# Performance work log

Hardware: AMD Instinct MI355X
Metric: run time of the kernel (lower is better)

The kernel has to match this reference:

```python
import jax, jax.numpy as jnp
import numpy as np

HIDDEN = 512
VOCAB = 50000
SEQ = 4096


def setup_inputs() -> dict:
    key = jax.random.key(0)
    ks = jax.random.split(key, 8)
    s = 1.0 / np.sqrt(HIDDEN)
    return {
        "x": jax.random.randint(ks[0], (1, SEQ), 0, VOCAB, dtype=jnp.int64),
        "target": jax.random.uniform(ks[1], (1, 1), dtype=jnp.float32),
        "emb": jax.random.normal(ks[2], (VOCAB, HIDDEN), dtype=jnp.float32),
        "w_ih": jax.random.uniform(ks[3], (3 * HIDDEN, HIDDEN), minval=-s, maxval=s, dtype=jnp.float32),
        "w_hh": jax.random.uniform(ks[4], (3 * HIDDEN, HIDDEN), minval=-s, maxval=s, dtype=jnp.float32),
        "b_ih": jax.random.uniform(ks[5], (3 * HIDDEN,), minval=-s, maxval=s, dtype=jnp.float32),
        "b_hh": jax.random.uniform(ks[6], (3 * HIDDEN,), minval=-s, maxval=s, dtype=jnp.float32),
        "dec_w": jax.random.uniform(ks[7], (1, HIDDEN), minval=-s, maxval=s, dtype=jnp.float32),
        "dec_b": jnp.zeros((1,), dtype=jnp.float32),
    }


def reference(x, target, emb, w_ih, w_hh, b_ih, b_hh, dec_w, dec_b):
    H = emb.shape[1]
    # embedding lookup for whole sequence (dropout in eval mode = identity)
    xe = emb[x[0]]                       # [S, H]
    # precompute input-side gate projections for all timesteps
    gx = xe @ w_ih.T + b_ih              # [S, 3H]

    def step(h, gx_t):
        gh = h @ w_hh.T + b_hh           # [3H]
        r = jax.nn.sigmoid(gx_t[:H] + gh[:H])
        z = jax.nn.sigmoid(gx_t[H:2 * H] + gh[H:2 * H])
        n = jnp.tanh(gx_t[2 * H:] + r * gh[2 * H:])
        h_new = (1.0 - z) * n + z * h
        return h_new, None

    h0 = jnp.zeros((H,), dtype=xe.dtype)
    hT, _ = jax.lax.scan(step, h0, gx)   # final hidden state [H]

    # decoder logit, then sigmoid + BCE (stable log-sigmoid form)
    logit = hT @ dec_w[0] + dec_b[0]     # scalar
    t = target[0, 0]
    loss = -(t * jax.nn.log_sigmoid(logit) + (1.0 - t) * jax.nn.log_sigmoid(-logit))
    return loss
```

## Files before the change

kernel.cpp:

```cpp
#include <hip/hip_runtime.h>

constexpr int S   = 4096;
constexpr int H   = 512;
constexpr int G3  = 1536;
constexpr int NWG = 32;

__global__ __launch_bounds__(256) void gemm_gx(
    const int* __restrict__ x, const float* __restrict__ emb,
    const float* __restrict__ w_ih, const float* __restrict__ b_ih,
    float* __restrict__ gx)
{
    __shared__ alignas(16) float As[128][36];
    __shared__ alignas(16) float Bs[32][132];

    const int tid  = threadIdx.x;
    const int row0 = (blockIdx.x / 12) * 128;
    const int col0 = (blockIdx.x % 12) * 128;
    const int tx   = tid & 15;
    const int ty   = tid >> 4;

    float acc[8][8] = {};

    for (int k0 = 0; k0 < H; k0 += 32) {
        #pragma unroll
        for (int p = 0; p < 4; ++p) {
            const int rl = (tid >> 3) + 32 * p;
            const int kk = (tid & 7) * 4;
            const int xi = x[row0 + rl];
            const float4 va = *reinterpret_cast<const float4*>(
                emb + (size_t)xi * H + k0 + kk);
            *reinterpret_cast<float4*>(&As[rl][kk]) = va;

            const float4 vb = *reinterpret_cast<const float4*>(
                w_ih + (size_t)(col0 + rl) * H + k0 + kk);
            Bs[kk + 0][rl] = vb.x; Bs[kk + 1][rl] = vb.y;
            Bs[kk + 2][rl] = vb.z; Bs[kk + 3][rl] = vb.w;
        }
        __syncthreads();

        #pragma unroll
        for (int kk = 0; kk < 32; ++kk) {
            float a[8], b[8];
            #pragma unroll
            for (int q = 0; q < 4; ++q) {
                a[q]     = As[ty * 4 + q][kk];
                a[4 + q] = As[ty * 4 + 64 + q][kk];
            }
            const float4 b0 = *reinterpret_cast<const float4*>(&Bs[kk][tx * 4]);
            const float4 b1 = *reinterpret_cast<const float4*>(&Bs[kk][tx * 4 + 64]);
            b[0]=b0.x; b[1]=b0.y; b[2]=b0.z; b[3]=b0.w;
            b[4]=b1.x; b[5]=b1.y; b[6]=b1.z; b[7]=b1.w;
            #pragma unroll
            for (int ri = 0; ri < 8; ++ri)
                #pragma unroll
                for (int ci = 0; ci < 8; ++ci)
                    acc[ri][ci] = fmaf(a[ri], b[ci], acc[ri][ci]);
        }
        __syncthreads();
    }

    float bi[8];
    #pragma unroll
    for (int q = 0; q < 4; ++q) {
        bi[q]     = b_ih[col0 + tx * 4 + q];
        bi[4 + q] = b_ih[col0 + tx * 4 + 64 + q];
    }
    #pragma unroll
    for (int ri = 0; ri < 8; ++ri) {
        const int rr = row0 + ty * 4 + (ri & 3) + ((ri >> 2) << 6);
        float4 o0, o1;
        o0.x = acc[ri][0] + bi[0]; o0.y = acc[ri][1] + bi[1];
        o0.z = acc[ri][2] + bi[2]; o0.w = acc[ri][3] + bi[3];
        o1.x = acc[ri][4] + bi[4]; o1.y = acc[ri][5] + bi[5];
        o1.z = acc[ri][6] + bi[6]; o1.w = acc[ri][7] + bi[7];
        *reinterpret_cast<float4*>(gx + (size_t)rr * G3 + col0 + tx * 4)      = o0;
        *reinterpret_cast<float4*>(gx + (size_t)rr * G3 + col0 + tx * 4 + 64) = o1;
    }
}

__global__ __launch_bounds__(256, 1) void gru_scan(
    const float* __restrict__ gx,
    const float* __restrict__ w_hh,
    const float* __restrict__ b_hh,
    const float* __restrict__ dec_w,
    const float* __restrict__ dec_b,
    const float* __restrict__ target,
    unsigned long long* __restrict__ hbuf,
    float* __restrict__ out)
{
    __shared__ float h_lds[H];

    const int k   = blockIdx.x;
    const int tid = threadIdx.x;
    const int l   = tid & 15;
    const int g   = tid >> 4;
    const int i   = k * 16 + g;

    float4 wr[8], wz[8], wn[8];
    #pragma unroll
    for (int j = 0; j < 8; ++j) {
        const int c = 4 * l + 64 * j;
        wr[j] = *reinterpret_cast<const float4*>(w_hh + (size_t)i * H + c);
        wz[j] = *reinterpret_cast<const float4*>(w_hh + (size_t)(H + i) * H + c);
        wn[j] = *reinterpret_cast<const float4*>(w_hh + (size_t)(2 * H + i) * H + c);
    }
    const float bhr = b_hh[i], bhz = b_hh[H + i], bhn = b_hh[2 * H + i];

    float gxr = 0.f, gxz = 0.f, gxn = 0.f;
    if (l == 0) { gxr = gx[i]; gxz = gx[H + i]; gxn = gx[2 * H + i]; }

    const int e0 = tid, e1 = tid + 256;

    for (int s = 0; s < S; ++s) {
        if (s == 0) {
            h_lds[e0] = 0.f; h_lds[e1] = 0.f;
        } else {
            unsigned long long* src = hbuf + (size_t)(s & 1) * H;
            unsigned long long v0 = 0, v1 = 0;
            bool d0 = false, d1 = false;
            const unsigned tg = (unsigned)s;
            while (true) {
                if (!d0) { v0 = __hip_atomic_load(src + e0, __ATOMIC_RELAXED,
                                                  __HIP_MEMORY_SCOPE_AGENT);
                           d0 = (unsigned)(v0 >> 32) == tg; }
                if (!d1) { v1 = __hip_atomic_load(src + e1, __ATOMIC_RELAXED,
                                                  __HIP_MEMORY_SCOPE_AGENT);
                           d1 = (unsigned)(v1 >> 32) == tg; }
                if (d0 && d1) break;
            }
            h_lds[e0] = __uint_as_float((unsigned)v0);
            h_lds[e1] = __uint_as_float((unsigned)v1);
        }
        __syncthreads();

        const float hp = h_lds[i];

        float ar = 0.f, az = 0.f, an = 0.f;
        #pragma unroll
        for (int j = 0; j < 8; ++j) {
            const float4 hv =
                *reinterpret_cast<const float4*>(&h_lds[64 * j + 4 * l]);
            ar = fmaf(wr[j].x, hv.x, fmaf(wr[j].y, hv.y,
                 fmaf(wr[j].z, hv.z, fmaf(wr[j].w, hv.w, ar))));
            az = fmaf(wz[j].x, hv.x, fmaf(wz[j].y, hv.y,
                 fmaf(wz[j].z, hv.z, fmaf(wz[j].w, hv.w, az))));
            an = fmaf(wn[j].x, hv.x, fmaf(wn[j].y, hv.y,
                 fmaf(wn[j].z, hv.z, fmaf(wn[j].w, hv.w, an))));
        }
        #pragma unroll
        for (int m = 8; m >= 1; m >>= 1) {
            ar += __shfl_xor(ar, m);
            az += __shfl_xor(az, m);
            an += __shfl_xor(an, m);
        }

        if (l == 0) {
            const float r  = 1.f / (1.f + __expf(-(gxr + ar + bhr)));
            const float z  = 1.f / (1.f + __expf(-(gxz + az + bhz)));
            const float nn = tanhf(gxn + r * (an + bhn));
            const float hnew = (1.f - z) * nn + z * hp;
            const unsigned long long pv =
                ((unsigned long long)(unsigned)(s + 1) << 32) |
                (unsigned long long)__float_as_uint(hnew);
            __hip_atomic_store(hbuf + (size_t)((s + 1) & 1) * H + i, pv,
                               __ATOMIC_RELAXED, __HIP_MEMORY_SCOPE_AGENT);
            const int sn = (s + 1 < S) ? (s + 1) : s;
            gxr = gx[(size_t)sn * G3 + i];
            gxz = gx[(size_t)sn * G3 + H + i];
            gxn = gx[(size_t)sn * G3 + 2 * H + i];
        }
        __syncthreads();
    }

    if (k == 0) {
        unsigned long long* src = hbuf;
        unsigned long long v0 = 0, v1 = 0;
        bool d0 = false, d1 = false;
        while (true) {
            if (!d0) { v0 = __hip_atomic_load(src + e0, __ATOMIC_RELAXED,
                                              __HIP_MEMORY_SCOPE_AGENT);
                       d0 = (unsigned)(v0 >> 32) == (unsigned)S; }
            if (!d1) { v1 = __hip_atomic_load(src + e1, __ATOMIC_RELAXED,
                                              __HIP_MEMORY_SCOPE_AGENT);
                       d1 = (unsigned)(v1 >> 32) == (unsigned)S; }
            if (d0 && d1) break;
        }
        h_lds[e0] = __uint_as_float((unsigned)v0);
        h_lds[e1] = __uint_as_float((unsigned)v1);
        __syncthreads();

        if (tid < 64) {
            float p = 0.f;
            #pragma unroll
            for (int j = 0; j < 8; ++j)
                p = fmaf(h_lds[tid + 64 * j], dec_w[tid + 64 * j], p);
            #pragma unroll
            for (int m = 32; m >= 1; m >>= 1) p += __shfl_xor(p, m);
            if (tid == 0) {
                const float xl = p + dec_b[0];
                const float t  = target[0];
                const float loss = fmaxf(xl, 0.f) - xl * t +
                                   log1pf(__expf(-fabsf(xl)));
                out[0] = loss;
            }
        }
    }
}

extern "C" void kernel_launch(void* const* d_in, const int* in_sizes, int n_in,
                              void* d_out, int out_size, void* d_ws, size_t ws_size,
                              hipStream_t stream) {
    const int*   x      = (const int*)d_in[0];
    const float* target = (const float*)d_in[1];
    const float* emb    = (const float*)d_in[2];
    const float* w_ih   = (const float*)d_in[3];
    const float* w_hh   = (const float*)d_in[4];
    const float* b_ih   = (const float*)d_in[5];
    const float* b_hh   = (const float*)d_in[6];
    const float* dec_w  = (const float*)d_in[7];
    const float* dec_b  = (const float*)d_in[8];
    float*       out    = (float*)d_out;

    float* gx = (float*)d_ws;
    unsigned long long* hbuf =
        (unsigned long long*)((char*)d_ws + (size_t)S * G3 * sizeof(float));

    hipMemsetAsync(hbuf, 0, 2 * H * sizeof(unsigned long long), stream);

    gemm_gx<<<dim3(32 * 12), dim3(256), 0, stream>>>(x, emb, w_ih, b_ih, gx);
    gru_scan<<<dim3(NWG), dim3(256), 0, stream>>>(gx, w_hh, b_hh, dec_w, dec_b,
                                                  target, hbuf, out);
}
```

Measured before the change: 8.090 ms.

## Co-locate scan workgroups on one XCD and exchange hidden state through L2

The scan kernel now launches 256 workgroups and keeps only every eighth one, so that under round-robin XCD dispatch all 32 active workgroups should sit on the same XCD. Each step publishes h both to an L2-coherent buffer, using sc0 inline-asm stores and loads, and to the original agent-scope buffer. Consumers poll the L2 buffer with vectorized 16-byte loads and fall back to the agent-scope buffer after a bounded spin. The trailing per-step __syncthreads is also dropped, aiming to cut the per-timestep cross-XCD communication latency that bounds the 4096-step recurrence. This relies on an undocumented workgroup-to-XCD placement and on the fallback path if that assumption fails.

```diff
diff --git a/kernel.cpp b/kernel.cpp
--- a/kernel.cpp
+++ b/kernel.cpp
@@ -1,9 +1,22 @@
 #include <hip/hip_runtime.h>
 
-constexpr int S   = 4096;
-constexpr int H   = 512;
-constexpr int G3  = 1536;
-constexpr int NWG = 32;
+constexpr int S    = 4096;
+constexpr int H    = 512;
+constexpr int G3   = 1536;
+constexpr int NWG  = 32;
+constexpr int GRID = 256;
+constexpr int FAST_BOUND = 16384;
+
+__device__ inline uint4 ld4_l2(const void* p) {
+    uint4 v;
+    asm volatile("global_load_dwordx4 %0, %1, off sc0\n\ts_waitcnt vmcnt(0)"
+                 : "=v"(v) : "v"(p) : "memory");
+    return v;
+}
+__device__ inline void st2_l2(void* p, unsigned long long v) {
+    asm volatile("global_store_dwordx2 %0, %1, off sc0"
+                 :: "v"(p), "v"(v) : "memory");
+}
 
 __global__ __launch_bounds__(256) void gemm_gx(
     const int* __restrict__ x, const float* __restrict__ emb,
@@ -85,51 +98,75 @@
     const float* __restrict__ dec_w,
     const float* __restrict__ dec_b,
     const float* __restrict__ target,
-    unsigned long long* __restrict__ hbuf,
+    unsigned long long* __restrict__ hl2,
+    unsigned long long* __restrict__ hml,
     float* __restrict__ out)
 {
+    const int bid = blockIdx.x;
+    if ((bid & 7) != 0) return;
+    const int k = bid >> 3;
+
     __shared__ float h_lds[H];
 
-    const int k   = blockIdx.x;
     const int tid = threadIdx.x;
     const int l   = tid & 15;
     const int g   = tid >> 4;
     const int i   = k * 16 + g;
+    const int e0  = 2 * tid, e1 = 2 * tid + 1;
 
     float4 wr[8], wz[8], wn[8];
     #pragma unroll
     for (int j = 0; j < 8; ++j) {
-        const int c = 4 * l + 64 * j;
-        wr[j] = *reinterpret_cast<const float4*>(w_hh + (size_t)i * H + c);
-        wz[j] = *reinterpret_cast<const float4*>(w_hh + (size_t)(H + i) * H + c);
-        wn[j] = *reinterpret_cast<const float4*>(w_hh + (size_t)(2 * H + i) * H + c);
+        const volatile float* pr =
+            (const volatile float*)(w_hh + (size_t)i * H + 4 * l + 64 * j);
+        const volatile float* pz = pr + (size_t)H * H;
+        const volatile float* pn = pz + (size_t)H * H;
+        wr[j] = make_float4(pr[0], pr[1], pr[2], pr[3]);
+        wz[j] = make_float4(pz[0], pz[1], pz[2], pz[3]);
+        wn[j] = make_float4(pn[0], pn[1], pn[2], pn[3]);
     }
     const float bhr = b_hh[i], bhz = b_hh[H + i], bhn = b_hh[2 * H + i];
 
     float gxr = 0.f, gxz = 0.f, gxn = 0.f;
     if (l == 0) { gxr = gx[i]; gxz = gx[H + i]; gxn = gx[2 * H + i]; }
 
-    const int e0 = tid, e1 = tid + 256;
+    bool use_mall = false;
 
     for (int s = 0; s < S; ++s) {
         if (s == 0) {
             h_lds[e0] = 0.f; h_lds[e1] = 0.f;
         } else {
-            unsigned long long* src = hbuf + (size_t)(s & 1) * H;
-            unsigned long long v0 = 0, v1 = 0;
-            bool d0 = false, d1 = false;
-            const unsigned tg = (unsigned)s;
-            while (true) {
-                if (!d0) { v0 = __hip_atomic_load(src + e0, __ATOMIC_RELAXED,
-                                                  __HIP_MEMORY_SCOPE_AGENT);
-                           d0 = (unsigned)(v0 >> 32) == tg; }
-                if (!d1) { v1 = __hip_atomic_load(src + e1, __ATOMIC_RELAXED,
-                                                  __HIP_MEMORY_SCOPE_AGENT);
-                           d1 = (unsigned)(v1 >> 32) == tg; }
-                if (d0 && d1) break;
-            }
-            h_lds[e0] = __uint_as_float((unsigned)v0);
-            h_lds[e1] = __uint_as_float((unsigned)v1);
+            const unsigned tg   = (unsigned)s;
+            const size_t   boff = (size_t)(s & 1) * H;
+            unsigned x0, x1;
+            bool got = false;
+            if (!use_mall) {
+                const uint4* src =
+                    reinterpret_cast<const uint4*>(hl2 + boff) + tid;
+                uint4 v = ld4_l2(src);
+                int it = 0;
+                while (!(v.y == tg && v.w == tg) && it < FAST_BOUND) {
+                    ++it; v = ld4_l2(src);
+                }
+                if (v.y == tg && v.w == tg) { x0 = v.x; x1 = v.z; got = true; }
+                else use_mall = true;
+            }
+            if (!got) {
+                unsigned long long* src = hml + boff;
+                unsigned long long v0 = 0, v1 = 0;
+                bool d0 = false, d1 = false;
+                while (!(d0 && d1)) {
+                    if (!d0) { v0 = __hip_atomic_load(src + e0, __ATOMIC_RELAXED,
+                                                      __HIP_MEMORY_SCOPE_AGENT);
+                               d0 = (unsigned)(v0 >> 32) == tg; }
+                    if (!d1) { v1 = __hip_atomic_load(src + e1, __ATOMIC_RELAXED,
+                                                      __HIP_MEMORY_SCOPE_AGENT);
+                               d1 = (unsigned)(v1 >> 32) == tg; }
+                }
+                x0 = (unsigned)v0; x1 = (unsigned)v1;
+            }
+            h_lds[e0] = __uint_as_float(x0);
+            h_lds[e1] = __uint_as_float(x1);
         }
         __syncthreads();
 
@@ -162,31 +199,46 @@
             const unsigned long long pv =
                 ((unsigned long long)(unsigned)(s + 1) << 32) |
                 (unsigned long long)__float_as_uint(hnew);
-            __hip_atomic_store(hbuf + (size_t)((s + 1) & 1) * H + i, pv,
+            const size_t dsts = (size_t)((s + 1) & 1) * H + i;
+            st2_l2(hl2 + dsts, pv);
+            __hip_atomic_store(hml + dsts, pv,
                                __ATOMIC_RELAXED, __HIP_MEMORY_SCOPE_AGENT);
             const int sn = (s + 1 < S) ? (s + 1) : s;
             gxr = gx[(size_t)sn * G3 + i];
             gxz = gx[(size_t)sn * G3 + H + i];
             gxn = gx[(size_t)sn * G3 + 2 * H + i];
         }
-        __syncthreads();
     }
 
     if (k == 0) {
-        unsigned long long* src = hbuf;
-        unsigned long long v0 = 0, v1 = 0;
-        bool d0 = false, d1 = false;
-        while (true) {
-            if (!d0) { v0 = __hip_atomic_load(src + e0, __ATOMIC_RELAXED,
-                                              __HIP_MEMORY_SCOPE_AGENT);
-                       d0 = (unsigned)(v0 >> 32) == (unsigned)S; }
-            if (!d1) { v1 = __hip_atomic_load(src + e1, __ATOMIC_RELAXED,
-                                              __HIP_MEMORY_SCOPE_AGENT);
-                       d1 = (unsigned)(v1 >> 32) == (unsigned)S; }
-            if (d0 && d1) break;
-        }
-        h_lds[e0] = __uint_as_float((unsigned)v0);
-        h_lds[e1] = __uint_as_float((unsigned)v1);
+        const unsigned tg = (unsigned)S;
+        unsigned x0, x1;
+        bool got = false;
+        if (!use_mall) {
+            const uint4* src = reinterpret_cast<const uint4*>(hl2) + tid;
+            uint4 v = ld4_l2(src);
+            int it = 0;
+            while (!(v.y == tg && v.w == tg) && it < FAST_BOUND) {
+                ++it; v = ld4_l2(src);
+            }
+            if (v.y == tg && v.w == tg) { x0 = v.x; x1 = v.z; got = true; }
+            else use_mall = true;
+        }
+        if (!got) {
+            unsigned long long v0 = 0, v1 = 0;
+            bool d0 = false, d1 = false;
+            while (!(d0 && d1)) {
+                if (!d0) { v0 = __hip_atomic_load(hml + e0, __ATOMIC_RELAXED,
+                                                  __HIP_MEMORY_SCOPE_AGENT);
+                           d0 = (unsigned)(v0 >> 32) == tg; }
+                if (!d1) { v1 = __hip_atomic_load(hml + e1, __ATOMIC_RELAXED,
+                                                  __HIP_MEMORY_SCOPE_AGENT);
+                           d1 = (unsigned)(v1 >> 32) == tg; }
+            }
+            x0 = (unsigned)v0; x1 = (unsigned)v1;
+        }
+        h_lds[e0] = __uint_as_float(x0);
+        h_lds[e1] = __uint_as_float(x1);
         __syncthreads();
 
         if (tid < 64) {
@@ -222,12 +274,13 @@
     float*       out    = (float*)d_out;
 
     float* gx = (float*)d_ws;
-    unsigned long long* hbuf =
+    unsigned long long* hl2 =
         (unsigned long long*)((char*)d_ws + (size_t)S * G3 * sizeof(float));
-
-    hipMemsetAsync(hbuf, 0, 2 * H * sizeof(unsigned long long), stream);
+    unsigned long long* hml = hl2 + 2 * H;
+
+    hipMemsetAsync(hl2, 0, 4 * H * sizeof(unsigned long long), stream);
 
     gemm_gx<<<dim3(32 * 12), dim3(256), 0, stream>>>(x, emb, w_ih, b_ih, gx);
-    gru_scan<<<dim3(NWG), dim3(256), 0, stream>>>(gx, w_hh, b_hh, dec_w, dec_b,
-                                                  target, hbuf, out);
-}
+    gru_scan<<<dim3(GRID), dim3(256), 0, stream>>>(gx, w_hh, b_hh, dec_w, dec_b,
+                                                   target, hl2, hml, out);
+}
```

New measurement: 25.23 ms. 212% more time.

## Poll hidden state with wide system-coherent loads and stage recurrent weights in LDS

Applied to the files above, without the earlier changes.

The per-step inter-workgroup handoff now polls 16 bytes per thread (two tagged entries) using an inline-asm global_load_dwordx4 with sc0 sc1 cache bits, and falls back to the original per-element atomic polling after a bounded number of tries. The aim is to cut the number of separate polls, and their latency, on the serial critical path. The recurrent weight slice moves from registers into a 96KB LDS buffer and the single-block occupancy bound is dropped, which lowers register pressure but adds LDS reads to every step. The inline asm waits on vmcnt(0) inside the poll loop and relies on the tag and value words landing coherently together within one 16-byte load.

```diff
diff --git a/kernel.cpp b/kernel.cpp
--- a/kernel.cpp
+++ b/kernel.cpp
@@ -4,6 +4,14 @@
 constexpr int H   = 512;
 constexpr int G3  = 1536;
 constexpr int NWG = 32;
+constexpr int FAST_TRIES = 256;
+
+__device__ inline uint4 ld4_mall(const void* p) {
+    uint4 v;
+    asm volatile("global_load_dwordx4 %0, %1, off sc0 sc1\n\ts_waitcnt vmcnt(0)"
+                 : "=v"(v) : "v"(p) : "memory");
+    return v;
+}
 
 __global__ __launch_bounds__(256) void gemm_gx(
     const int* __restrict__ x, const float* __restrict__ emb,
@@ -78,7 +86,7 @@
     }
 }
 
-__global__ __launch_bounds__(256, 1) void gru_scan(
+__global__ __launch_bounds__(256) void gru_scan(
     const float* __restrict__ gx,
     const float* __restrict__ w_hh,
     const float* __restrict__ b_hh,
@@ -88,7 +96,8 @@
     unsigned long long* __restrict__ hbuf,
     float* __restrict__ out)
 {
-    __shared__ float h_lds[H];
+    __shared__ alignas(16) float w_lds[3 * 16 * 512];
+    __shared__ alignas(16) float h_lds[H];
 
     const int k   = blockIdx.x;
     const int tid = threadIdx.x;
@@ -96,40 +105,63 @@
     const int g   = tid >> 4;
     const int i   = k * 16 + g;
 
-    float4 wr[8], wz[8], wn[8];
     #pragma unroll
-    for (int j = 0; j < 8; ++j) {
-        const int c = 4 * l + 64 * j;
-        wr[j] = *reinterpret_cast<const float4*>(w_hh + (size_t)i * H + c);
-        wz[j] = *reinterpret_cast<const float4*>(w_hh + (size_t)(H + i) * H + c);
-        wn[j] = *reinterpret_cast<const float4*>(w_hh + (size_t)(2 * H + i) * H + c);
-    }
+    for (int m = 0; m < 24; ++m) {
+        const int p = tid + 256 * m;
+        const int q = p >> 11;
+        const int r = (p >> 7) & 15;
+        const int c = p & 127;
+        const float4 v = *reinterpret_cast<const float4*>(
+            w_hh + ((size_t)q * H + k * 16 + r) * H + 4 * c);
+        *reinterpret_cast<float4*>(&w_lds[((q * 16 + r) << 9) + 4 * c]) = v;
+    }
+
     const float bhr = b_hh[i], bhz = b_hh[H + i], bhn = b_hh[2 * H + i];
 
     float gxr = 0.f, gxz = 0.f, gxn = 0.f;
     if (l == 0) { gxr = gx[i]; gxz = gx[H + i]; gxn = gx[2 * H + i]; }
-
-    const int e0 = tid, e1 = tid + 256;
+    __syncthreads();
+
+    const float* wr_ = &w_lds[((0 * 16 + g) << 9) + 4 * l];
+    const float* wz_ = &w_lds[((1 * 16 + g) << 9) + 4 * l];
+    const float* wn_ = &w_lds[((2 * 16 + g) << 9) + 4 * l];
+
+    bool slow = false;
 
     for (int s = 0; s < S; ++s) {
         if (s == 0) {
-            h_lds[e0] = 0.f; h_lds[e1] = 0.f;
+            h_lds[2 * tid] = 0.f; h_lds[2 * tid + 1] = 0.f;
         } else {
-            unsigned long long* src = hbuf + (size_t)(s & 1) * H;
-            unsigned long long v0 = 0, v1 = 0;
-            bool d0 = false, d1 = false;
-            const unsigned tg = (unsigned)s;
-            while (true) {
-                if (!d0) { v0 = __hip_atomic_load(src + e0, __ATOMIC_RELAXED,
-                                                  __HIP_MEMORY_SCOPE_AGENT);
-                           d0 = (unsigned)(v0 >> 32) == tg; }
-                if (!d1) { v1 = __hip_atomic_load(src + e1, __ATOMIC_RELAXED,
-                                                  __HIP_MEMORY_SCOPE_AGENT);
-                           d1 = (unsigned)(v1 >> 32) == tg; }
-                if (d0 && d1) break;
-            }
-            h_lds[e0] = __uint_as_float((unsigned)v0);
-            h_lds[e1] = __uint_as_float((unsigned)v1);
+            const unsigned tg   = (unsigned)s;
+            const size_t   boff = (size_t)(s & 1) * H;
+            unsigned x0, x1;
+            bool got = false;
+            if (!slow) {
+                const void* src = (const char*)(hbuf + boff) + 16 * (size_t)tid;
+                uint4 v = ld4_mall(src);
+                int it = 0;
+                while (!(v.y == tg && v.w == tg) && it < FAST_TRIES) {
+                    ++it; v = ld4_mall(src);
+                }
+                if (v.y == tg && v.w == tg) { x0 = v.x; x1 = v.z; got = true; }
+                else slow = true;
+            }
+            if (!got) {
+                unsigned long long* src = hbuf + boff;
+                unsigned long long v0 = 0, v1 = 0;
+                bool d0 = false, d1 = false;
+                while (!(d0 && d1)) {
+                    if (!d0) { v0 = __hip_atomic_load(src + 2 * tid,
+                                   __ATOMIC_RELAXED, __HIP_MEMORY_SCOPE_AGENT);
+                               d0 = (unsigned)(v0 >> 32) == tg; }
+                    if (!d1) { v1 = __hip_atomic_load(src + 2 * tid + 1,
+                                   __ATOMIC_RELAXED, __HIP_MEMORY_SCOPE_AGENT);
+                               d1 = (unsigned)(v1 >> 32) == tg; }
+                }
+                x0 = (unsigned)v0; x1 = (unsigned)v1;
+            }
+            h_lds[2 * tid]     = __uint_as_float(x0);
+            h_lds[2 * tid + 1] = __uint_as_float(x1);
         }
         __syncthreads();
 
@@ -138,14 +170,13 @@
         float ar = 0.f, az = 0.f, an = 0.f;
         #pragma unroll
         for (int j = 0; j < 8; ++j) {
-            const float4 hv =
-                *reinterpret_cast<const float4*>(&h_lds[64 * j + 4 * l]);
-            ar = fmaf(wr[j].x, hv.x, fmaf(wr[j].y, hv.y,
-                 fmaf(wr[j].z, hv.z, fmaf(wr[j].w, hv.w, ar))));
-            az = fmaf(wz[j].x, hv.x, fmaf(wz[j].y, hv.y,
-                 fmaf(wz[j].z, hv.z, fmaf(wz[j].w, hv.w, az))));
-            an = fmaf(wn[j].x, hv.x, fmaf(wn[j].y, hv.y,
-                 fmaf(wn[j].z, hv.z, fmaf(wn[j].w, hv.w, an))));
+            const float4 hv = *reinterpret_cast<const float4*>(&h_lds[64 * j + 4 * l]);
+            const float4 a  = *reinterpret_cast<const float4*>(wr_ + 64 * j);
+            const float4 b  = *reinterpret_cast<const float4*>(wz_ + 64 * j);
+            const float4 c  = *reinterpret_cast<const float4*>(wn_ + 64 * j);
+            ar = fmaf(a.x, hv.x, fmaf(a.y, hv.y, fmaf(a.z, hv.z, fmaf(a.w, hv.w, ar))));
+            az = fmaf(b.x, hv.x, fmaf(b.y, hv.y, fmaf(b.z, hv.z, fmaf(b.w, hv.w, az))));
+            an = fmaf(c.x, hv.x, fmaf(c.y, hv.y, fmaf(c.z, hv.z, fmaf(c.w, hv.w, an))));
         }
         #pragma unroll
         for (int m = 8; m >= 1; m >>= 1) {
@@ -173,20 +204,18 @@
     }
 
     if (k == 0) {
-        unsigned long long* src = hbuf;
         unsigned long long v0 = 0, v1 = 0;
         bool d0 = false, d1 = false;
-        while (true) {
-            if (!d0) { v0 = __hip_atomic_load(src + e0, __ATOMIC_RELAXED,
-                                              __HIP_MEMORY_SCOPE_AGENT);
+        while (!(d0 && d1)) {
+            if (!d0) { v0 = __hip_atomic_load(hbuf + 2 * tid,
+                           __ATOMIC_RELAXED, __HIP_MEMORY_SCOPE_AGENT);
                        d0 = (unsigned)(v0 >> 32) == (unsigned)S; }
-            if (!d1) { v1 = __hip_atomic_load(src + e1, __ATOMIC_RELAXED,
-                                              __HIP_MEMORY_SCOPE_AGENT);
+            if (!d1) { v1 = __hip_atomic_load(hbuf + 2 * tid + 1,
+                           __ATOMIC_RELAXED, __HIP_MEMORY_SCOPE_AGENT);
                        d1 = (unsigned)(v1 >> 32) == (unsigned)S; }
-            if (d0 && d1) break;
-        }
-        h_lds[e0] = __uint_as_float((unsigned)v0);
-        h_lds[e1] = __uint_as_float((unsigned)v1);
+        }
+        h_lds[2 * tid]     = __uint_as_float((unsigned)v0);
+        h_lds[2 * tid + 1] = __uint_as_float((unsigned)v1);
         __syncthreads();
 
         if (tid < 64) {
```

After: 9.392 ms. 16.1% more time.
